# Kernel optimization log

Measured on AMD Instinct MI355X. Metric: run time of the kernel, lower is better.

The kernel has to match this reference:

```python
import math
import jax, jax.numpy as jnp
import numpy as np

B = 128          # graphs per batch
N = 1024         # nodes per graph
E = 1048576      # total edges (avg degree 8)
F_IN = 64
NHID = 64
NCLS = 10
RATIO = 0.8


def setup_inputs() -> dict:
    key = jax.random.key(0)
    ks = jax.random.split(key, 24)
    x = jax.random.normal(ks[0], (B * N, F_IN), jnp.float32)
    # intra-graph random edges: graph id per edge, local src/dst
    epg = E // B
    gid = jnp.repeat(jnp.arange(B, dtype=jnp.int32), epg)
    src = gid * N + jax.random.randint(ks[1], (E,), 0, N, jnp.int32)
    dst = gid * N + jax.random.randint(ks[2], (E,), 0, N, jnp.int32)
    def lin(k, fi, fo):
        s = 1.0 / np.sqrt(fi)
        return jax.random.uniform(k, (fi, fo), jnp.float32, -s, s)
    p = {
        'W1': lin(ks[3], F_IN, NHID), 'b1': jnp.zeros((NHID,), jnp.float32),
        'Wp1': lin(ks[4], NHID, 1), 'bp1': jnp.zeros((1,), jnp.float32),
        'W2': lin(ks[5], NHID, NHID), 'b2': jnp.zeros((NHID,), jnp.float32),
        'Wp2': lin(ks[6], NHID, 1), 'bp2': jnp.zeros((1,), jnp.float32),
        'W3': lin(ks[7], NHID, NHID), 'b3': jnp.zeros((NHID,), jnp.float32),
        'Wp3': lin(ks[8], NHID, 1), 'bp3': jnp.zeros((1,), jnp.float32),
        'L1w': lin(ks[9], 2 * NHID, NHID), 'L1b': jnp.zeros((NHID,), jnp.float32),
        'L2w': lin(ks[10], NHID, NHID // 2), 'L2b': jnp.zeros((NHID // 2,), jnp.float32),
        'L3w': lin(ks[11], NHID // 2, NCLS), 'L3b': jnp.zeros((NCLS,), jnp.float32),
    }
    return dict(x=x, edge_src=src, edge_dst=dst, **p)


def gcn_conv(x, W, b, src, dst, emask, n):
    # PyG GCNConv: add self loops, symmetric deg normalization
    xw = x @ W
    ew = emask.astype(x.dtype)
    deg = jax.ops.segment_sum(ew, dst, num_segments=n) + 1.0  # +1 self loop
    dis = jax.lax.rsqrt(deg)
    norm = dis[src] * dis[dst] * ew
    agg = jax.ops.segment_sum(xw[src] * norm[:, None], dst, num_segments=n)
    agg = agg + xw * (dis * dis)[:, None]  # self-loop message
    return agg + b


def sag_pool(x, Wp, bp, src, dst, emask, n_cur):
    n_tot = B * n_cur
    k = int(math.ceil(RATIO * n_cur))
    score = gcn_conv(x, Wp, bp, src, dst, emask, n_tot)[:, 0]
    _, idx = jax.lax.top_k(score.reshape(B, n_cur), k)
    perm = (idx + (jnp.arange(B, dtype=jnp.int32) * n_cur)[:, None]).reshape(-1)
    xn = x[perm] * jnp.tanh(score[perm])[:, None]
    new_idx = jnp.full((n_tot,), -1, jnp.int32).at[perm].set(
        jnp.arange(B * k, dtype=jnp.int32))
    ns, nd = new_idx[src], new_idx[dst]
    valid = emask & (ns >= 0) & (nd >= 0)
    return xn, jnp.where(valid, ns, 0), jnp.where(valid, nd, 0), valid, k


def readout(x, k):
    xr = x.reshape(B, k, NHID)
    return jnp.concatenate([xr.max(axis=1), xr.mean(axis=1)], axis=1)


def reference(x, edge_src, edge_dst, W1, b1, Wp1, bp1, W2, b2, Wp2, bp2,
              W3, b3, Wp3, bp3, L1w, L1b, L2w, L2b, L3w, L3b):
    src = edge_src.astype(jnp.int32)
    dst = edge_dst.astype(jnp.int32)
    emask = jnp.ones((E,), bool)
    n = N
    h = jax.nn.relu(gcn_conv(x, W1, b1, src, dst, emask, B * n))
    h, src, dst, emask, n = sag_pool(h, Wp1, bp1, src, dst, emask, n)
    r1 = readout(h, n)
    h = jax.nn.relu(gcn_conv(h, W2, b2, src, dst, emask, B * n))
    h, src, dst, emask, n = sag_pool(h, Wp2, bp2, src, dst, emask, n)
    r2 = readout(h, n)
    h = jax.nn.relu(gcn_conv(h, W3, b3, src, dst, emask, B * n))
    h, src, dst, emask, n = sag_pool(h, Wp3, bp3, src, dst, emask, n)
    r3 = readout(h, n)
    z = r1 + r2 + r3
    z = jax.nn.relu(z @ L1w + L1b)          # dropout is identity in eval
    z = jax.nn.relu(z @ L2w + L2b)
    return jax.nn.log_softmax(z @ L3w + L3b, axis=-1)
```

## Files before the change

kernel.cpp:

```cpp
#include <hip/hip_runtime.h>
#include <math.h>

constexpr int B_  = 128;
constexpr int N_  = 1024;
constexpr int E_  = 1048576;
constexpr int BN_ = B_ * N_;
constexpr int EPG = E_ / B_;
constexpr int NSEG = 16;

typedef short v8s __attribute__((ext_vector_type(8)));
typedef float v4f __attribute__((ext_vector_type(4)));

__device__ __forceinline__ unsigned bf16_rne(unsigned u) {
    return (u + 0x7FFFu + ((u >> 16) & 1u)) >> 16;
}

__global__ __launch_bounds__(1024) void k_csr2(
        const int* __restrict__ src, const int* __restrict__ dst,
        const int* __restrict__ cum,
        int* __restrict__ srt, int* __restrict__ rowptr,
        float* __restrict__ dis, int n) {
    __shared__ int cnt[1024];
    __shared__ int cur[1024];
    __shared__ int cums[1024];
    __shared__ int wsum[17];
    int g = blockIdx.x, tid = threadIdx.x;
    int gb   = g * N_;
    int base = g * n;
    const int eb = g * EPG;

    cums[tid] = cum ? cum[gb + tid] : tid;
    cnt[tid] = 0;
    __syncthreads();
    for (int t = tid; t < EPG; t += 1024) {
        int s = cums[src[eb + t] - gb];
        int d = cums[dst[eb + t] - gb];
        if ((s | d) >= 0) atomicAdd(&cnt[d], 1);
    }
    __syncthreads();

    int c = (tid < n) ? cnt[tid] : 0;
    int v = c;
    int lane = tid & 63, wv = tid >> 6;
    #pragma unroll
    for (int off = 1; off < 64; off <<= 1) {
        int t = __shfl_up(v, off, 64);
        if (lane >= off) v += t;
    }
    if (lane == 63) wsum[wv] = v;
    __syncthreads();
    if (tid == 0) {
        int run = 0;
        #pragma unroll
        for (int i = 0; i < 16; ++i) { int t = wsum[i]; wsum[i] = run; run += t; }
        wsum[16] = run;
    }
    __syncthreads();
    int excl = v - c + wsum[wv];
    if (tid < n) {
        cur[tid] = excl;
        rowptr[g * (n + 1) + tid] = excl;
        dis[base + tid] = rsqrtf((float)c + 1.0f);
    }
    if (tid == 0) rowptr[g * (n + 1) + n] = wsum[16];
    __syncthreads();

    for (int t = tid; t < EPG; t += 1024) {
        int s = cums[src[eb + t] - gb];
        int d = cums[dst[eb + t] - gb];
        if ((s | d) < 0) continue;
        int pos = atomicAdd(&cur[d], 1);
        srt[eb + pos] = s;
    }
}

__global__ __launch_bounds__(1024) void k_wprep3(
        const float* __restrict__ W0, const float* __restrict__ W1,
        const float* __restrict__ W2, unsigned short* __restrict__ wfall) {
    const float* W = (blockIdx.x == 0) ? W0 : (blockIdx.x == 1) ? W1 : W2;
    unsigned short* wf = wfall + (size_t)blockIdx.x * 8192;
    int t = threadIdx.x;
    int l  = t & 63;
    int kk = (t >> 6) & 1;
    int c  = (t >> 7) & 3;
    int p  = (t >> 9) & 1;
    int col = c * 16 + (l & 15);
    int kbase = kk * 32 + (l >> 4) * 8;
    unsigned short o[8];
    #pragma unroll
    for (int j = 0; j < 8; ++j) {
        float w = W[(kbase + j) * 64 + col];
        unsigned u  = __float_as_uint(w);
        unsigned hi = bf16_rne(u);
        if (p == 0) o[j] = (unsigned short)hi;
        else {
            float lo = w - __uint_as_float(hi << 16);
            o[j] = (unsigned short)bf16_rne(__float_as_uint(lo));
        }
    }
    uint4 v;
    v.x = o[0] | ((unsigned)o[1] << 16);
    v.y = o[2] | ((unsigned)o[3] << 16);
    v.z = o[4] | ((unsigned)o[5] << 16);
    v.w = o[6] | ((unsigned)o[7] << 16);
    *reinterpret_cast<uint4*>(wf + (size_t)t * 8) = v;
}

__global__ __launch_bounds__(256) void k_xw_mfma(
        const float* __restrict__ h, const int* __restrict__ perm,
        const float* __restrict__ ggate, const unsigned short* __restrict__ wf,
        const float* __restrict__ dis, float* __restrict__ xwq, int rows) {
    __shared__ float hs[128][68];
    __shared__ float sdis[128];
    __shared__ int   lperm[128];
    __shared__ float lgate[128];
    int tid = threadIdx.x;
    int r0 = blockIdx.x * 128;

    if (perm) {
        if (tid < 128) { lperm[tid] = perm[r0 + tid]; lgate[tid] = ggate[r0 + tid]; }
        __syncthreads();
        for (int i = tid; i < 128 * 16; i += 256) {
            int row = i >> 4, s = i & 15;
            float4 v = *reinterpret_cast<const float4*>(h + (size_t)lperm[row] * 64 + s * 4);
            float gt = lgate[row];
            v.x *= gt; v.y *= gt; v.z *= gt; v.w *= gt;
            *reinterpret_cast<float4*>(&hs[row][s * 4]) = v;
        }
    } else {
        for (int i = tid; i < 128 * 16; i += 256) {
            int row = i >> 4, s = i & 15;
            float4 v = *reinterpret_cast<const float4*>(h + (size_t)(r0 + row) * 64 + s * 4);
            *reinterpret_cast<float4*>(&hs[row][s * 4]) = v;
        }
    }
    if (tid < 128) sdis[tid] = dis[r0 + tid];

    int lane = tid & 63;
    v8s wh[4][2], wl[4][2];
    #pragma unroll
    for (int c = 0; c < 4; ++c) {
        #pragma unroll
        for (int kk = 0; kk < 2; ++kk) {
            wh[c][kk] = *reinterpret_cast<const v8s*>(wf + (((size_t)((0*4 + c)*2 + kk))*64 + lane)*8);
            wl[c][kk] = *reinterpret_cast<const v8s*>(wf + (((size_t)((1*4 + c)*2 + kk))*64 + lane)*8);
        }
    }
    __syncthreads();

    int wave = tid >> 6;
    int m = lane & 15, b = lane >> 4;
    #pragma unroll
    for (int t = 0; t < 2; ++t) {
        int lr0 = (wave * 2 + t) * 16;
        float f[16];
        *reinterpret_cast<float4*>(f)      = *reinterpret_cast<const float4*>(&hs[lr0 + m][b * 8]);
        *reinterpret_cast<float4*>(f + 4)  = *reinterpret_cast<const float4*>(&hs[lr0 + m][b * 8 + 4]);
        *reinterpret_cast<float4*>(f + 8)  = *reinterpret_cast<const float4*>(&hs[lr0 + m][32 + b * 8]);
        *reinterpret_cast<float4*>(f + 12) = *reinterpret_cast<const float4*>(&hs[lr0 + m][32 + b * 8 + 4]);
        v8s ah[2], al[2];
        #pragma unroll
        for (int ch = 0; ch < 2; ++ch) {
            #pragma unroll
            for (int j = 0; j < 8; ++j) {
                float x = f[ch * 8 + j];
                unsigned u  = __float_as_uint(x);
                unsigned hi = bf16_rne(u);
                float lo = x - __uint_as_float(hi << 16);
                ah[ch][j] = (short)hi;
                al[ch][j] = (short)bf16_rne(__float_as_uint(lo));
            }
        }
        float dv[4];
        #pragma unroll
        for (int reg = 0; reg < 4; ++reg) dv[reg] = sdis[lr0 + b * 4 + reg];

        #pragma unroll
        for (int c = 0; c < 4; ++c) {
            v4f acc = {0.f, 0.f, 0.f, 0.f};
            acc = __builtin_amdgcn_mfma_f32_16x16x32_bf16(ah[0], wh[c][0], acc, 0, 0, 0);
            acc = __builtin_amdgcn_mfma_f32_16x16x32_bf16(ah[1], wh[c][1], acc, 0, 0, 0);
            acc = __builtin_amdgcn_mfma_f32_16x16x32_bf16(al[0], wh[c][0], acc, 0, 0, 0);
            acc = __builtin_amdgcn_mfma_f32_16x16x32_bf16(al[1], wh[c][1], acc, 0, 0, 0);
            acc = __builtin_amdgcn_mfma_f32_16x16x32_bf16(ah[0], wl[c][0], acc, 0, 0, 0);
            acc = __builtin_amdgcn_mfma_f32_16x16x32_bf16(ah[1], wl[c][1], acc, 0, 0, 0);
            acc = __builtin_amdgcn_mfma_f32_16x16x32_bf16(al[0], wl[c][0], acc, 0, 0, 0);
            acc = __builtin_amdgcn_mfma_f32_16x16x32_bf16(al[1], wl[c][1], acc, 0, 0, 0);
            #pragma unroll
            for (int reg = 0; reg < 4; ++reg) {
                int grow = r0 + lr0 + b * 4 + reg;
                xwq[((size_t)c * rows + grow) * 16 + m] = acc[reg] * dv[reg];
            }
        }
    }
}

__global__ __launch_bounds__(1024) void k_agg_csr(
        const int* __restrict__ srt, const int* __restrict__ rowptr,
        const float* __restrict__ dis, const float* __restrict__ xwq,
        const float* __restrict__ bias, const float* __restrict__ Wp,
        float* __restrict__ hout, float* __restrict__ sxwsq,
        int n, int rows) {
    extern __shared__ float lds[];
    float* xs  = lds;
    int* lsrt  = (int*)(lds + n * 20);
    int* lrp   = lsrt + EPG;
    int g = blockIdx.x >> 2, q = blockIdx.x & 3;
    int foff = q * 16;
    int tid  = threadIdx.x;
    int base = g * n;
    const float* plane = xwq + ((size_t)q * rows + base) * 16;

    for (int i = tid; i < n * 4; i += 1024) {
        int row = i >> 2, sub = i & 3;
        float4 v = *reinterpret_cast<const float4*>(plane + row * 16 + sub * 4);
        *reinterpret_cast<float4*>(xs + row * 20 + sub * 4) = v;
    }
    for (int i = tid; i <= n; i += 1024) lrp[i] = rowptr[g * (n + 1) + i];
    __syncthreads();
    int total = lrp[n];
    const int* gsrt = srt + g * EPG;
    for (int i = tid; i < total; i += 1024) lsrt[i] = gsrt[i];
    __syncthreads();

    int sub = tid & 3;
    float4 b   = *reinterpret_cast<const float4*>(bias + foff + sub * 4);
    float4 wp4 = *reinterpret_cast<const float4*>(Wp   + foff + sub * 4);
    for (int row = tid >> 2; row < n; row += 256) {
        int s0 = lrp[row], s1 = lrp[row + 1];
        float4 acc = *reinterpret_cast<const float4*>(xs + row * 20 + sub * 4);
        for (int j = s0; j < s1; ++j) {
            int s = lsrt[j];
            const float4 v = *reinterpret_cast<const float4*>(xs + s * 20 + sub * 4);
            acc.x += v.x; acc.y += v.y; acc.z += v.z; acc.w += v.w;
        }
        float dsc = dis[base + row];
        float4 o;
        o.x = fmaxf(fmaf(dsc, acc.x, b.x), 0.0f);
        o.y = fmaxf(fmaf(dsc, acc.y, b.y), 0.0f);
        o.z = fmaxf(fmaf(dsc, acc.z, b.z), 0.0f);
        o.w = fmaxf(fmaf(dsc, acc.w, b.w), 0.0f);
        *reinterpret_cast<float4*>(hout + (size_t)(base + row) * 64 + foff + sub * 4) = o;
        float part = o.x * wp4.x + o.y * wp4.y + o.z * wp4.z + o.w * wp4.w;
        part += __shfl_xor(part, 1, 64);
        part += __shfl_xor(part, 2, 64);
        if (sub == 0) sxwsq[(size_t)q * BN_ + base + row] = part;
    }
}

__global__ __launch_bounds__(1024) void k_score_topk(
        const int* __restrict__ srt, const int* __restrict__ rowptr,
        const float* __restrict__ dis, const float* __restrict__ sxwsq,
        const float* __restrict__ bp, int n, int k,
        int* __restrict__ perm, float* __restrict__ ggate,
        int* __restrict__ cum, int do_compose) {
    __shared__ float xs[1024];
    __shared__ int   lrp[1025];
    __shared__ int   lsrt[EPG];
    unsigned long long* keys = (unsigned long long*)lsrt;
    int* mark = (int*)xs;
    int g = blockIdx.x, tid = threadIdx.x;
    int base = g * n;
    float bp0 = bp[0];

    if (tid < n) {
        float s0 = sxwsq[0 * (size_t)BN_ + base + tid] + sxwsq[1 * (size_t)BN_ + base + tid]
                 + sxwsq[2 * (size_t)BN_ + base + tid] + sxwsq[3 * (size_t)BN_ + base + tid];
        xs[tid] = s0 * dis[base + tid];
    }
    for (int i = tid; i <= n; i += 1024) lrp[i] = rowptr[g * (n + 1) + i];
    __syncthreads();
    int total = lrp[n];
    for (int i = tid; i < total; i += 1024) lsrt[i] = srt[g * EPG + i];
    __syncthreads();

    float sag = 0.0f;
    if (tid < n) {
        float acc = xs[tid];
        int s1 = lrp[tid + 1];
        for (int j = lrp[tid]; j < s1; ++j) acc += xs[lsrt[j]];
        sag = dis[base + tid] * acc + bp0;
    }
    __syncthreads();

    {
        unsigned long long kv = 0ull;
        if (tid < n) {
            unsigned u  = __float_as_uint(sag);
            unsigned mk = (u & 0x80000000u) ? ~u : (u | 0x80000000u);
            kv = ((unsigned long long)mk << 32) | (unsigned)tid;
        }
        keys[tid] = kv;
        mark[tid] = -1;
    }

    for (int size = 2; size <= 1024; size <<= 1) {
        for (int stride = size >> 1; stride > 0; stride >>= 1) {
            __syncthreads();
            if (tid < 512) {
                int a  = ((tid / stride) * (stride << 1)) + (tid & (stride - 1));
                int bx = a + stride;
                bool asc = ((a & size) == 0);
                unsigned long long ka = keys[a], kb = keys[bx];
                bool sw = asc ? (ka > kb) : (ka < kb);
                if (sw) { keys[a] = kb; keys[bx] = ka; }
            }
        }
    }
    __syncthreads();

    if (tid < k) {
        int j = tid;
        unsigned long long kv = keys[1023 - j];
        int local   = (int)(kv & 0xFFFFFFFFull);
        unsigned mk = (unsigned)(kv >> 32);
        unsigned u  = (mk & 0x80000000u) ? (mk ^ 0x80000000u) : ~mk;
        int newg = g * k + j;
        perm[newg]  = base + local;
        ggate[newg] = tanhf(__uint_as_float(u));
        mark[local] = j;
    }
    __syncthreads();
    if (do_compose) {
        int gb = g * N_;
        int c = (do_compose == 1) ? tid : cum[gb + tid];
        cum[gb + tid] = (c >= 0) ? mark[c] : -1;
    }
}

__global__ __launch_bounds__(256) void k_readout_seg(
        const float* __restrict__ h, const int* __restrict__ perm,
        const float* __restrict__ ggate, int k, float* __restrict__ pz) {
    int g = blockIdx.x / NSEG, seg = blockIdx.x % NSEG;
    int ck = (k + NSEG - 1) / NSEG;
    int j0 = seg * ck;
    int j1 = min(k, j0 + ck);
    __shared__ float gate[64];
    __shared__ int   lperm[64];
    int tid = threadIdx.x;
    for (int j = j0 + tid; j < j1; j += 256) {
        lperm[j - j0] = perm[g * k + j];
        gate[j - j0]  = ggate[g * k + j];
    }
    __syncthreads();
    int lane = tid & 63, w = tid >> 6;
    float mx = -INFINITY, sm = 0.0f;
    for (int j = j0 + w; j < j1; j += 4) {
        float v = h[(size_t)lperm[j - j0] * 64 + lane] * gate[j - j0];
        mx = fmaxf(mx, v); sm += v;
    }
    __shared__ float smx[4][64], ssm[4][64];
    smx[w][lane] = mx; ssm[w][lane] = sm;
    __syncthreads();
    if (w == 0) {
        #pragma unroll
        for (int i = 1; i < 4; ++i) { mx = fmaxf(mx, smx[i][lane]); sm += ssm[i][lane]; }
        float* p = pz + ((size_t)g * NSEG + seg) * 128;
        p[lane]      = mx;
        p[64 + lane] = sm;
    }
}

__global__ __launch_bounds__(128) void k_mlp(const float* __restrict__ pz,
                      const float* __restrict__ L1w, const float* __restrict__ L1b,
                      const float* __restrict__ L2w, const float* __restrict__ L2b,
                      const float* __restrict__ L3w, const float* __restrict__ L3b,
                      float* __restrict__ out) {
    __shared__ float z[128], h1[64], h2[32], lg[10], lse;
    int g = blockIdx.x, tid = threadIdx.x;
    const float kinv[3] = {1.0f / 820.0f, 1.0f / 656.0f, 1.0f / 525.0f};
    float zv = 0.0f;
    if (tid < 64) {
        #pragma unroll
        for (int L = 0; L < 3; ++L) {
            const float* p = pz + (((size_t)L * B_ + g) * NSEG) * 128;
            float mx = -INFINITY;
            #pragma unroll
            for (int s = 0; s < NSEG; ++s) mx = fmaxf(mx, p[s * 128 + tid]);
            zv += mx;
        }
    } else {
        int f = tid - 64;
        #pragma unroll
        for (int L = 0; L < 3; ++L) {
            const float* p = pz + (((size_t)L * B_ + g) * NSEG) * 128;
            float sm = 0.0f;
            #pragma unroll
            for (int s = 0; s < NSEG; ++s) sm += p[s * 128 + 64 + f];
            zv += sm * kinv[L];
        }
    }
    z[tid] = zv;
    __syncthreads();
    if (tid < 64) {
        float acc = L1b[tid];
        for (int i = 0; i < 128; ++i) acc = fmaf(z[i], L1w[i * 64 + tid], acc);
        h1[tid] = fmaxf(acc, 0.0f);
    }
    __syncthreads();
    if (tid < 32) {
        float acc = L2b[tid];
        for (int i = 0; i < 64; ++i) acc = fmaf(h1[i], L2w[i * 32 + tid], acc);
        h2[tid] = fmaxf(acc, 0.0f);
    }
    __syncthreads();
    if (tid < 10) {
        float acc = L3b[tid];
        for (int i = 0; i < 32; ++i) acc = fmaf(h2[i], L3w[i * 10 + tid], acc);
        lg[tid] = acc;
    }
    __syncthreads();
    if (tid == 0) {
        float m = lg[0];
        for (int i = 1; i < 10; ++i) m = fmaxf(m, lg[i]);
        float s = 0.0f;
        for (int i = 0; i < 10; ++i) s += expf(lg[i] - m);
        lse = m + logf(s);
    }
    __syncthreads();
    if (tid < 10) out[g * 10 + tid] = lg[tid] - lse;
}

extern "C" void kernel_launch(void* const* d_in, const int* in_sizes, int n_in,
                              void* d_out, int out_size, void* d_ws, size_t ws_size,
                              hipStream_t stream) {
    const float* x    = (const float*)d_in[0];
    const int*   esrc = (const int*)d_in[1];
    const int*   edst = (const int*)d_in[2];
    const float* W [3] = {(const float*)d_in[3],  (const float*)d_in[7],  (const float*)d_in[11]};
    const float* bb[3] = {(const float*)d_in[4],  (const float*)d_in[8],  (const float*)d_in[12]};
    const float* Wp[3] = {(const float*)d_in[5],  (const float*)d_in[9],  (const float*)d_in[13]};
    const float* bp[3] = {(const float*)d_in[6],  (const float*)d_in[10], (const float*)d_in[14]};
    const float* L1w = (const float*)d_in[15];
    const float* L1b = (const float*)d_in[16];
    const float* L2w = (const float*)d_in[17];
    const float* L2b = (const float*)d_in[18];
    const float* L3w = (const float*)d_in[19];
    const float* L3b = (const float*)d_in[20];
    float* out = (float*)d_out;

    float* fws   = (float*)d_ws;
    float* agg   = fws;
    float* xwq   = agg  + (size_t)BN_ * 64;
    float* dis   = xwq  + (size_t)BN_ * 64;
    float* sxwsq = dis  + BN_;
    float* ggate = sxwsq + 4 * (size_t)BN_;
    float* pz    = ggate + BN_;
    int*   perm   = (int*)(pz + 3 * B_ * NSEG * 128);
    int*   cum    = perm + BN_;
    int*   srt    = cum + BN_;
    int*   rowptr = srt + E_;
    unsigned short* wfrag = (unsigned short*)(rowptr + B_ * (N_ + 1));

    hipFuncSetAttribute(reinterpret_cast<const void*>(k_agg_csr),
                        hipFuncAttributeMaxDynamicSharedMemorySize,
                        (1024 * 20 + EPG + 1025) * 4);

    k_wprep3<<<3, 1024, 0, stream>>>(W[0], W[1], W[2], wfrag);

    const int ks_[3] = {820, 656, 525};
    int n = N_;

    for (int L = 0; L < 3; ++L) {
        int rows = B_ * n;
        int k    = ks_[L];

        k_csr2<<<B_, 1024, 0, stream>>>(esrc, edst, (L == 0) ? nullptr : cum,
                                        srt, rowptr, dis, n);

        if (L == 0)
            k_xw_mfma<<<rows / 128, 256, 0, stream>>>(x, nullptr, nullptr,
                                                      wfrag, dis, xwq, rows);
        else
            k_xw_mfma<<<rows / 128, 256, 0, stream>>>(agg, perm, ggate,
                                                      wfrag + (size_t)L * 8192, dis, xwq, rows);

        k_agg_csr<<<B_ * 4, 1024, (size_t)(n * 20 + EPG + n + 1) * 4, stream>>>(
            srt, rowptr, dis, xwq, bb[L], Wp[L], agg, sxwsq, n, rows);

        k_score_topk<<<B_, 1024, 0, stream>>>(srt, rowptr, dis, sxwsq, bp[L], n, k,
                                              perm, ggate, cum, (L < 2) ? (L + 1) : 0);

        k_readout_seg<<<B_ * NSEG, 256, 0, stream>>>(agg, perm, ggate, k,
                                                     pz + (size_t)L * B_ * NSEG * 128);

        n = k;
    }

    k_mlp<<<B_, 128, 0, stream>>>(pz, L1w, L1b, L2w, L2b, L3w, L3b, out);
}
```

Baseline: 226.6 us.

## Split GCN aggregation into two 32-feature halves with 16-bit LDS indices

The feature layout produced by the MFMA transform changes from four 16-wide planes to two 32-wide planes. The aggregation kernel now runs 256 blocks, each handling half the features of one graph, with a 32-lane group per row doing scalar gathers instead of 4-lane float4 gathers. Edge indices and row pointers are stored in LDS as unsigned shorts so a full 32-wide slice fits, and the dis scaling of the score partial moves into the aggregation kernel. The goal is to halve the redundant CSR loads and block count, at the cost of larger per-block LDS and one block per CU.

```diff
diff --git a/kernel.cpp b/kernel.cpp
--- a/kernel.cpp
+++ b/kernel.cpp
@@ -109,7 +109,7 @@
 __global__ __launch_bounds__(256) void k_xw_mfma(
         const float* __restrict__ h, const int* __restrict__ perm,
         const float* __restrict__ ggate, const unsigned short* __restrict__ wf,
-        const float* __restrict__ dis, float* __restrict__ xwq, int rows) {
+        const float* __restrict__ dis, float* __restrict__ xwh, int rows) {
     __shared__ float hs[128][68];
     __shared__ float sdis[128];
     __shared__ int   lperm[128];
@@ -189,68 +189,62 @@
             #pragma unroll
             for (int reg = 0; reg < 4; ++reg) {
                 int grow = r0 + lr0 + b * 4 + reg;
-                xwq[((size_t)c * rows + grow) * 16 + m] = acc[reg] * dv[reg];
+                xwh[((size_t)(c >> 1) * rows + grow) * 32 + (c & 1) * 16 + m] = acc[reg] * dv[reg];
             }
         }
     }
 }
 
-__global__ __launch_bounds__(1024) void k_agg_csr(
+__global__ __launch_bounds__(1024, 1) void k_agg_half(
         const int* __restrict__ srt, const int* __restrict__ rowptr,
-        const float* __restrict__ dis, const float* __restrict__ xwq,
+        const float* __restrict__ dis, const float* __restrict__ xwh,
         const float* __restrict__ bias, const float* __restrict__ Wp,
-        float* __restrict__ hout, float* __restrict__ sxwsq,
+        float* __restrict__ hout, float* __restrict__ sxwsh,
         int n, int rows) {
-    extern __shared__ float lds[];
-    float* xs  = lds;
-    int* lsrt  = (int*)(lds + n * 20);
-    int* lrp   = lsrt + EPG;
-    int g = blockIdx.x >> 2, q = blockIdx.x & 3;
-    int foff = q * 16;
+    extern __shared__ float xs[];
+    unsigned short* lsrtU = (unsigned short*)(xs + n * 32);
+    unsigned short* lrpU  = lsrtU + EPG;
+
+    int g = blockIdx.x & 127, hf = blockIdx.x >> 7;
     int tid  = threadIdx.x;
     int base = g * n;
-    const float* plane = xwq + ((size_t)q * rows + base) * 16;
-
-    for (int i = tid; i < n * 4; i += 1024) {
-        int row = i >> 2, sub = i & 3;
-        float4 v = *reinterpret_cast<const float4*>(plane + row * 16 + sub * 4);
-        *reinterpret_cast<float4*>(xs + row * 20 + sub * 4) = v;
-    }
-    for (int i = tid; i <= n; i += 1024) lrp[i] = rowptr[g * (n + 1) + i];
-    __syncthreads();
-    int total = lrp[n];
+    const float* plane = xwh + ((size_t)hf * rows + base) * 32;
+    const int* grp = rowptr + g * (n + 1);
+
+    for (int i = tid; i < n * 8; i += 1024) {
+        float4 v = *reinterpret_cast<const float4*>(plane + i * 4);
+        *reinterpret_cast<float4*>(xs + i * 4) = v;
+    }
+    for (int i = tid; i <= n; i += 1024) lrpU[i] = (unsigned short)grp[i];
+    int total = grp[n];
     const int* gsrt = srt + g * EPG;
-    for (int i = tid; i < total; i += 1024) lsrt[i] = gsrt[i];
-    __syncthreads();
-
-    int sub = tid & 3;
-    float4 b   = *reinterpret_cast<const float4*>(bias + foff + sub * 4);
-    float4 wp4 = *reinterpret_cast<const float4*>(Wp   + foff + sub * 4);
-    for (int row = tid >> 2; row < n; row += 256) {
-        int s0 = lrp[row], s1 = lrp[row + 1];
-        float4 acc = *reinterpret_cast<const float4*>(xs + row * 20 + sub * 4);
+    for (int i = tid; i < total; i += 1024) lsrtU[i] = (unsigned short)gsrt[i];
+    __syncthreads();
+
+    int lane31 = tid & 31;
+    int hw = tid >> 5;
+    float bq  = bias[hf * 32 + lane31];
+    float wpl = Wp[hf * 32 + lane31];
+    for (int row = hw; row < n; row += 32) {
+        int s0 = lrpU[row], s1 = lrpU[row + 1];
+        float acc = xs[row * 32 + lane31];
         for (int j = s0; j < s1; ++j) {
-            int s = lsrt[j];
-            const float4 v = *reinterpret_cast<const float4*>(xs + s * 20 + sub * 4);
-            acc.x += v.x; acc.y += v.y; acc.z += v.z; acc.w += v.w;
+            int s = lsrtU[j];
+            acc += xs[s * 32 + lane31];
         }
         float dsc = dis[base + row];
-        float4 o;
-        o.x = fmaxf(fmaf(dsc, acc.x, b.x), 0.0f);
-        o.y = fmaxf(fmaf(dsc, acc.y, b.y), 0.0f);
-        o.z = fmaxf(fmaf(dsc, acc.z, b.z), 0.0f);
-        o.w = fmaxf(fmaf(dsc, acc.w, b.w), 0.0f);
-        *reinterpret_cast<float4*>(hout + (size_t)(base + row) * 64 + foff + sub * 4) = o;
-        float part = o.x * wp4.x + o.y * wp4.y + o.z * wp4.z + o.w * wp4.w;
-        part += __shfl_xor(part, 1, 64);
-        part += __shfl_xor(part, 2, 64);
-        if (sub == 0) sxwsq[(size_t)q * BN_ + base + row] = part;
+        float o = fmaxf(fmaf(dsc, acc, bq), 0.0f);
+        hout[(size_t)(base + row) * 64 + hf * 32 + lane31] = o;
+        float part = o * wpl;
+        #pragma unroll
+        for (int off = 16; off; off >>= 1) part += __shfl_xor(part, off, 32);
+        if (lane31 == 0) sxwsh[(size_t)hf * BN_ + base + row] = part * dsc;
     }
 }
 
 __global__ __launch_bounds__(1024) void k_score_topk(
         const int* __restrict__ srt, const int* __restrict__ rowptr,
-        const float* __restrict__ dis, const float* __restrict__ sxwsq,
+        const float* __restrict__ dis, const float* __restrict__ sxwsh,
         const float* __restrict__ bp, int n, int k,
         int* __restrict__ perm, float* __restrict__ ggate,
         int* __restrict__ cum, int do_compose) {
@@ -264,9 +258,8 @@
     float bp0 = bp[0];
 
     if (tid < n) {
-        float s0 = sxwsq[0 * (size_t)BN_ + base + tid] + sxwsq[1 * (size_t)BN_ + base + tid]
-                 + sxwsq[2 * (size_t)BN_ + base + tid] + sxwsq[3 * (size_t)BN_ + base + tid];
-        xs[tid] = s0 * dis[base + tid];
+        float s0 = sxwsh[0 * (size_t)BN_ + base + tid] + sxwsh[1 * (size_t)BN_ + base + tid];
+        xs[tid] = s0;
     }
     for (int i = tid; i <= n; i += 1024) lrp[i] = rowptr[g * (n + 1) + i];
     __syncthreads();
@@ -441,10 +434,10 @@
 
     float* fws   = (float*)d_ws;
     float* agg   = fws;
-    float* xwq   = agg  + (size_t)BN_ * 64;
-    float* dis   = xwq  + (size_t)BN_ * 64;
-    float* sxwsq = dis  + BN_;
-    float* ggate = sxwsq + 4 * (size_t)BN_;
+    float* xwh   = agg  + (size_t)BN_ * 64;
+    float* dis   = xwh  + (size_t)BN_ * 64;
+    float* sxwsh = dis  + BN_;
+    float* ggate = sxwsh + 4 * (size_t)BN_;
     float* pz    = ggate + BN_;
     int*   perm   = (int*)(pz + 3 * B_ * NSEG * 128);
     int*   cum    = perm + BN_;
@@ -452,9 +445,9 @@
     int*   rowptr = srt + E_;
     unsigned short* wfrag = (unsigned short*)(rowptr + B_ * (N_ + 1));
 
-    hipFuncSetAttribute(reinterpret_cast<const void*>(k_agg_csr),
+    hipFuncSetAttribute(reinterpret_cast<const void*>(k_agg_half),
                         hipFuncAttributeMaxDynamicSharedMemorySize,
-                        (1024 * 20 + EPG + 1025) * 4);
+                        1024 * 32 * 4 + EPG * 2 + 1026 * 2);
 
     k_wprep3<<<3, 1024, 0, stream>>>(W[0], W[1], W[2], wfrag);
 
@@ -470,15 +463,16 @@
 
         if (L == 0)
             k_xw_mfma<<<rows / 128, 256, 0, stream>>>(x, nullptr, nullptr,
-                                                      wfrag, dis, xwq, rows);
+                                                      wfrag, dis, xwh, rows);
         else
             k_xw_mfma<<<rows / 128, 256, 0, stream>>>(agg, perm, ggate,
-                                                      wfrag + (size_t)L * 8192, dis, xwq, rows);
-
-        k_agg_csr<<<B_ * 4, 1024, (size_t)(n * 20 + EPG + n + 1) * 4, stream>>>(
-            srt, rowptr, dis, xwq, bb[L], Wp[L], agg, sxwsq, n, rows);
-
-        k_score_topk<<<B_, 1024, 0, stream>>>(srt, rowptr, dis, sxwsq, bp[L], n, k,
+                                                      wfrag + (size_t)L * 8192, dis, xwh, rows);
+
+        size_t ldsB = (size_t)n * 32 * 4 + (size_t)EPG * 2 + (size_t)(n + 2) * 2;
+        k_agg_half<<<B_ * 2, 1024, ldsB, stream>>>(
+            srt, rowptr, dis, xwh, bb[L], Wp[L], agg, sxwsh, n, rows);
+
+        k_score_topk<<<B_, 1024, 0, stream>>>(srt, rowptr, dis, sxwsh, bp[L], n, k,
                                               perm, ggate, cum, (L < 2) ? (L + 1) : 0);
 
         k_readout_seg<<<B_ * NSEG, 256, 0, stream>>>(agg, perm, ggate, k,
```

Result: slower. 265.5 us (+17.2%).
